# Kernel optimization log

Measured on AMD Instinct MI355X. Metric: run time of the kernel, lower is better.

## Reference

```python
import jax, jax.numpy as jnp
import numpy as np

N_NODES = 4096
N_EDGES = 16384
F_IN = 64
F_EDGE = 16
HID = 128
OUT = 64
N_GRAPHS = 32


def _encoder(x, edge_index, edge_attr, batch, p):
    N = x.shape[0]
    src, dst = edge_index[0], edge_index[1]
    # EdgeMLP: [E, F_edge] -> [E, F_in * HID] per-edge weight matrices
    h = jax.nn.relu(edge_attr @ p['e_w1'] + p['e_b1'])
    h = jax.nn.relu(h @ p['e_w2'] + p['e_b2'])
    Wmat = (h @ p['e_w3'] + p['e_b3']).reshape(-1, x.shape[1], p['root_w'].shape[1])  # [E, F_in, HID]
    # NNConv: message = x_src @ W_edge, scatter-add to dst, plus root transform + bias
    msg = jnp.einsum('ei,eio->eo', x[src], Wmat)  # [E, HID]
    agg = jax.ops.segment_sum(msg, dst, num_segments=N)
    h1 = jax.nn.relu(agg + x @ p['root_w'] + p['conv1_b'])  # [N, HID]
    # GATConv (1 head, concat=False) with self-loops (PyG default)
    loop = jnp.arange(N, dtype=src.dtype)
    si = jnp.concatenate([src, loop])
    di = jnp.concatenate([dst, loop])
    hp = h1 @ p['gat_w']  # [N, HID]
    a_s = hp @ p['att_src']  # [N]
    a_d = hp @ p['att_dst']  # [N]
    e = jax.nn.leaky_relu(a_s[si] + a_d[di], negative_slope=0.2)
    m = jax.ops.segment_max(e, di, num_segments=N)
    ex = jnp.exp(e - m[di])
    denom = jax.ops.segment_sum(ex, di, num_segments=N)
    alpha = ex / (denom[di] + 1e-16)
    h2 = jax.ops.segment_sum(alpha[:, None] * hp[si], di, num_segments=N) + p['gat_b']
    h2 = jax.nn.relu(h2)
    # global mean pool over graphs
    s = jax.ops.segment_sum(h2, batch, num_segments=N_GRAPHS)
    cnt = jax.ops.segment_sum(jnp.ones((N,), h2.dtype), batch, num_segments=N_GRAPHS)
    pooled = s / jnp.maximum(cnt, 1.0)[:, None]
    return jax.nn.relu(pooled @ p['fc1_w'] + p['fc1_b'])  # [B, OUT]


def setup_inputs() -> dict:
    key = jax.random.key(0)
    ks = jax.random.split(key, 24)
    d = {}
    d['x1'] = jax.random.normal(ks[0], (N_NODES, F_IN), jnp.float32)
    d['edge_index1'] = jax.random.randint(ks[1], (2, N_EDGES), 0, N_NODES)
    d['edge_attr1'] = jax.random.normal(ks[2], (N_EDGES, F_EDGE), jnp.float32)
    d['batch1'] = jnp.sort(jax.random.randint(ks[3], (N_NODES,), 0, N_GRAPHS))
    d['x2'] = jax.random.normal(ks[4], (N_NODES, F_IN), jnp.float32)
    d['edge_index2'] = jax.random.randint(ks[5], (2, N_EDGES), 0, N_NODES)
    d['edge_attr2'] = jax.random.normal(ks[6], (N_EDGES, F_EDGE), jnp.float32)
    d['batch2'] = jnp.sort(jax.random.randint(ks[7], (N_NODES,), 0, N_GRAPHS))

    def lin(k, fi, fo):
        return jax.random.normal(k, (fi, fo), jnp.float32) * (fi ** -0.5)

    d['e_w1'] = lin(ks[8], F_EDGE, 128); d['e_b1'] = jnp.zeros((128,), jnp.float32)
    d['e_w2'] = lin(ks[9], 128, 64); d['e_b2'] = jnp.zeros((64,), jnp.float32)
    d['e_w3'] = lin(ks[10], 64, F_IN * HID); d['e_b3'] = jnp.zeros((F_IN * HID,), jnp.float32)
    d['root_w'] = lin(ks[11], F_IN, HID); d['conv1_b'] = jnp.zeros((HID,), jnp.float32)
    d['gat_w'] = lin(ks[12], HID, HID)
    d['att_src'] = jax.random.normal(ks[13], (HID,), jnp.float32) * (HID ** -0.5)
    d['att_dst'] = jax.random.normal(ks[14], (HID,), jnp.float32) * (HID ** -0.5)
    d['gat_b'] = jnp.zeros((HID,), jnp.float32)
    d['fc1_w'] = lin(ks[15], HID, OUT); d['fc1_b'] = jnp.zeros((OUT,), jnp.float32)
    d['fc2_w'] = lin(ks[16], OUT, 1); d['fc2_b'] = jnp.zeros((1,), jnp.float32)
    return d


def reference(x1, edge_index1, edge_attr1, batch1, x2, edge_index2, edge_attr2, batch2,
              e_w1, e_b1, e_w2, e_b2, e_w3, e_b3, root_w, conv1_b,
              gat_w, att_src, att_dst, gat_b, fc1_w, fc1_b, fc2_w, fc2_b):
    p = dict(e_w1=e_w1, e_b1=e_b1, e_w2=e_w2, e_b2=e_b2, e_w3=e_w3, e_b3=e_b3,
             root_w=root_w, conv1_b=conv1_b, gat_w=gat_w, att_src=att_src,
             att_dst=att_dst, gat_b=gat_b, fc1_w=fc1_w, fc1_b=fc1_b,
             fc2_w=fc2_w, fc2_b=fc2_b)
    z1 = _encoder(x1, edge_index1, edge_attr1, batch1, p)
    z2 = _encoder(x2, edge_index2, edge_attr2, batch2, p)
    z = jnp.abs(z1 - z2) @ fc2_w + fc2_b  # [B, 1]
    return jax.nn.sigmoid(z).squeeze(1)  # [B]
```

## Files before the change

kernel.cpp:

```cpp
#include <hip/hip_runtime.h>
#include <hip/hip_bf16.h>
#include <math.h>

#define NN 4096
#define NE 16384
#define FIN 64
#define FE 16
#define HIDD 128
#define OUTD 64
#define NG 32
#define EP (NE + NN)
#define KSPLIT 2
#define NCH (64 / KSPLIT)

typedef __attribute__((ext_vector_type(8))) short s8v;
typedef __attribute__((ext_vector_type(4))) unsigned u4v;
typedef __attribute__((ext_vector_type(4))) float f4v;

union FragU { u4v u; s8v s; };

__device__ __forceinline__ unsigned bf16_rne(float v) {
    unsigned b = __float_as_uint(v);
    return (b + 0x7FFFu + ((b >> 16) & 1u)) >> 16;
}

__device__ __forceinline__ void glds16(const void* g, void* l) {
    __builtin_amdgcn_global_load_lds(
        (const __attribute__((address_space(1))) unsigned*)g,
        (__attribute__((address_space(3))) unsigned*)l, 16, 0, 0);
}

#define PB_SPLIT 2048
#define PB_EMLP  (PB_SPLIT + 4096)
#define PB_BIAS  (PB_EMLP + 4096)
#define PB_TOTAL (PB_BIAS + 32)

__global__ void k_prep(const float* __restrict__ ea0, const float* __restrict__ ea1,
                       const float* __restrict__ w1, const float* __restrict__ b1,
                       const float* __restrict__ w2, const float* __restrict__ b2,
                       const float* __restrict__ w3,
                       const float* __restrict__ X0, const float* __restrict__ X1,
                       const float* __restrict__ b3,
                       const int* __restrict__ ei0, const int* __restrict__ ei1,
                       unsigned short* __restrict__ B1g, unsigned short* __restrict__ B2g,
                       float* __restrict__ h0, float* __restrict__ h1g,
                       float* __restrict__ Bb0, float* __restrict__ Bb1,
                       int* __restrict__ rowcnt) {
    int b = blockIdx.x, t = threadIdx.x;
    if (b < PB_SPLIT) {
        int g = b * 256 + t;
        int o = g & 127, i = (g >> 7) & 63, c = g >> 13;
        float v = w3[(size_t)c * 8192 + i * 128 + o];
        unsigned hi = __float_as_uint(v) & 0xFFFF0000u;
        float res = v - __uint_as_float(hi);
        unsigned r2 = bf16_rne(res);
        unsigned idx = ((unsigned)c << 13) + (((o << 6) + i) ^ ((o & 7) << 3));
        B1g[idx] = (unsigned short)(hi >> 16);
        B2g[idx] = (unsigned short)r2;
    } else if (b < PB_EMLP) {
        int bb = b - PB_SPLIT;
        int gi = bb >> 11;
        int e0 = (bb & 2047) * 8;
        const float* ea = gi ? ea1 : ea0;
        float* hout = gi ? h1g : h0;
        __shared__ float h1s[8][HIDD];
#pragma unroll
        for (int r = 0; r < 4; ++r) {
            int idx = r * 256 + t;
            int e1 = idx >> 7, j = idx & 127;
            float acc = b1[j];
#pragma unroll
            for (int i = 0; i < FE; ++i) acc += ea[(e0 + e1) * FE + i] * w1[i * HIDD + j];
            h1s[e1][j] = fmaxf(acc, 0.f);
        }
        __syncthreads();
#pragma unroll
        for (int r = 0; r < 2; ++r) {
            int idx = r * 256 + t;
            int e1 = idx >> 6, j = idx & 63;
            float acc = b2[j];
#pragma unroll 16
            for (int k = 0; k < HIDD; ++k) acc += h1s[e1][k] * w2[k * 64 + j];
            hout[(size_t)(e0 + e1) * 64 + j] = fmaxf(acc, 0.f);
        }
    } else if (b < PB_BIAS) {
        int bb = b - PB_EMLP;
        int gi = bb >> 11;
        int n = (bb & 2047) * 2 + (t >> 7);
        int o = t & 127;
        const float* X = gi ? X1 : X0;
        float* Bb = gi ? Bb1 : Bb0;
        float acc = 0.f;
#pragma unroll 16
        for (int i = 0; i < FIN; ++i) acc += X[n * FIN + i] * b3[i * HIDD + o];
        Bb[(size_t)n * HIDD + o] = acc;
    } else {
        int tid = (b - PB_BIAS) * 256 + t;
        for (int idx = tid; idx < 2 * EP; idx += 32 * 256) {
            int gi = idx / EP, e = idx % EP;
            const int* dst = (gi ? ei1 : ei0) + NE;
            int d = (e < NE) ? dst[e] : e - NE;
            atomicAdd(&rowcnt[gi * NN + d], 1);
        }
    }
}

__global__ void k_scan(const int* __restrict__ rowcnt, int* __restrict__ rowptr,
                       const int* __restrict__ batch0, const int* __restrict__ batch1,
                       int* __restrict__ br) {
    int b = blockIdx.x;
    if (b < 2) {
        int gi = b;
        const int* cnt = rowcnt + gi * NN;
        int* rp = rowptr + gi * (NN + 1);
        int t = threadIdx.x;
        int base = t * 4;
        int v0 = cnt[base], v1 = cnt[base + 1], v2 = cnt[base + 2], v3 = cnt[base + 3];
        int s = v0 + v1 + v2 + v3;
        __shared__ int sc[1024];
        sc[t] = s;
        __syncthreads();
        for (int off = 1; off < 1024; off <<= 1) {
            int a = (t >= off) ? sc[t - off] : 0;
            __syncthreads();
            sc[t] += a;
            __syncthreads();
        }
        int run = sc[t] - s;
        rp[base] = run; run += v0;
        rp[base + 1] = run; run += v1;
        rp[base + 2] = run; run += v2;
        rp[base + 3] = run; run += v3;
        if (t == 1023) rp[NN] = run;
    } else {
        int t = threadIdx.x;
        if (t < 66) {
            int gi = t / 33, g = t % 33;
            const int* batch = gi ? batch1 : batch0;
            int lo = 0, hi = NN;
            while (lo < hi) {
                int mid = (lo + hi) >> 1;
                if (batch[mid] < g) lo = mid + 1; else hi = mid;
            }
            br[gi * 33 + g] = lo;
        }
    }
}

__global__ void k_fill(const int* __restrict__ ei0, const int* __restrict__ ei1,
                       const int* __restrict__ rowptr, int* __restrict__ cnt2,
                       int* __restrict__ adj) {
    int idx = blockIdx.x * 256 + threadIdx.x;
    if (idx >= 2 * EP) return;
    int gi = idx / EP, e = idx % EP;
    const int* dst = (gi ? ei1 : ei0) + NE;
    int d = (e < NE) ? dst[e] : e - NE;
    int pos = rowptr[gi * (NN + 1) + d] + atomicAdd(&cnt2[gi * NN + d], 1);
    adj[gi * EP + pos] = e;
}

__global__ void __launch_bounds__(256, 2)
k_nnconv(const float* __restrict__ x0, const float* __restrict__ x1,
         const float* __restrict__ h_0, const float* __restrict__ h_1,
         const unsigned short* __restrict__ B1g, const unsigned short* __restrict__ B2g,
         const float* __restrict__ Bb0, const float* __restrict__ Bb1,
         const int* __restrict__ ei0, const int* __restrict__ ei1,
         float* __restrict__ msg) {
    __shared__ __align__(16) char smem[65536];
    int gi = blockIdx.z;
    const float* x = gi ? x1 : x0;
    const float* hh = gi ? h_1 : h_0;
    const float* Bb = gi ? Bb1 : Bb0;
    const int* src = gi ? ei1 : ei0;

    int t = threadIdx.x;
    int e0 = blockIdx.x * 128;
    int z = blockIdx.y;
    int wv = t >> 6, l = t & 63;
    int q4 = l >> 4, c16 = l & 15;

    float xs[2][16];
    float hs[2][NCH];
#pragma unroll
    for (int mf = 0; mf < 2; ++mf) {
        int r = wv * 32 + mf * 16 + c16;
        int s_ = src[e0 + r];
        const float* xr = &x[(size_t)s_ * FIN];
        *(float4*)&xs[mf][0]  = *(const float4*)&xr[q4 * 8];
        *(float4*)&xs[mf][4]  = *(const float4*)&xr[q4 * 8 + 4];
        *(float4*)&xs[mf][8]  = *(const float4*)&xr[32 + q4 * 8];
        *(float4*)&xs[mf][12] = *(const float4*)&xr[32 + q4 * 8 + 4];
        const float* hr = &hh[(size_t)(e0 + r) * 64 + z * NCH];
#pragma unroll
        for (int q = 0; q < NCH / 4; ++q)
            *(float4*)&hs[mf][q * 4] = *(const float4*)&hr[q * 4];
    }

    f4v acc[2][8];
#pragma unroll
    for (int a = 0; a < 2; ++a)
#pragma unroll
        for (int b = 0; b < 8; ++b) acc[a][b] = (f4v){0.f, 0.f, 0.f, 0.f};

    int woff = wv << 10;
#define STAGE(cg, buf)                                                         \
    {                                                                          \
        const char* b1src = (const char*)B1g + (size_t)(cg) * 16384;           \
        const char* b2src = (const char*)B2g + (size_t)(cg) * 16384;           \
        char* B1s_ = smem + (buf) * 32768;                                     \
        char* B2s_ = B1s_ + 16384;                                             \
        _Pragma("unroll")                                                      \
        for (int k2 = 0; k2 < 4; ++k2) {                                       \
            glds16(b1src + k2 * 4096 + t * 16, B1s_ + k2 * 4096 + woff);       \
            glds16(b2src + k2 * 4096 + t * 16, B2s_ + k2 * 4096 + woff);       \
        }                                                                      \
    }

    STAGE(z * NCH, 0);

#pragma unroll 1
    for (int cl = 0; cl < NCH; ++cl) {
        int buf = cl & 1;
        __builtin_amdgcn_s_barrier();
        __builtin_amdgcn_sched_barrier(0);
        if (cl + 1 < NCH) STAGE(z * NCH + cl + 1, buf ^ 1);

        FragU a1[2][2], a2[2][2];
#pragma unroll
        for (int mf = 0; mf < 2; ++mf) {
            float hv = hs[mf][cl];
#pragma unroll
            for (int kf = 0; kf < 2; ++kf) {
                u4v w1v, w2v;
#pragma unroll
                for (int p = 0; p < 4; ++p) {
                    float p0 = hv * xs[mf][kf * 8 + 2 * p];
                    float p1 = hv * xs[mf][kf * 8 + 2 * p + 1];
                    unsigned b0 = __float_as_uint(p0), b1 = __float_as_uint(p1);
                    unsigned hi0 = b0 & 0xFFFF0000u, hi1 = b1 & 0xFFFF0000u;
                    w1v[p] = (hi0 >> 16) | hi1;
                    float r0 = p0 - __uint_as_float(hi0);
                    float r1 = p1 - __uint_as_float(hi1);
                    w2v[p] = bf16_rne(r0) | (bf16_rne(r1) << 16);
                }
                a1[mf][kf].u = w1v; a2[mf][kf].u = w2v;
            }
        }

        if (cl + 1 < NCH) { asm volatile("s_waitcnt vmcnt(8)" ::: "memory"); }
        else             { asm volatile("s_waitcnt vmcnt(0)" ::: "memory"); }
        __builtin_amdgcn_sched_barrier(0);
        __builtin_amdgcn_s_barrier();
        __builtin_amdgcn_sched_barrier(0);

        const char* B1s = smem + buf * 32768;
        const char* B2s = B1s + 16384;
        __builtin_amdgcn_s_setprio(1);
#pragma unroll
        for (int kf = 0; kf < 2; ++kf) {
#pragma unroll
            for (int nf = 0; nf < 8; ++nf) {
                int o = nf * 16 + c16;
                int byte = o * 128 + ((kf * 64 + q4 * 16) ^ ((o & 7) << 4));
                FragU bf1, bf2;
                bf1.u = *(const u4v*)(B1s + byte);
                bf2.u = *(const u4v*)(B2s + byte);
#pragma unroll
                for (int mf = 0; mf < 2; ++mf) {
                    acc[mf][nf] = __builtin_amdgcn_mfma_f32_16x16x32_bf16(a1[mf][kf].s, bf1.s, acc[mf][nf], 0, 0, 0);
                    acc[mf][nf] = __builtin_amdgcn_mfma_f32_16x16x32_bf16(a1[mf][kf].s, bf2.s, acc[mf][nf], 0, 0, 0);
                    acc[mf][nf] = __builtin_amdgcn_mfma_f32_16x16x32_bf16(a2[mf][kf].s, bf1.s, acc[mf][nf], 0, 0, 0);
                }
            }
        }
        __builtin_amdgcn_s_setprio(0);
    }
#undef STAGE

    float* sm = (float*)smem;
    float* mb = msg + ((size_t)(gi * KSPLIT + z) * NE) * HIDD;
    int z0 = (z == 0);
#pragma unroll
    for (int half = 0; half < 2; ++half) {
        __syncthreads();
        if ((wv >> 1) == half) {
            int rbase = (wv & 1) * 32;
#pragma unroll
            for (int mf = 0; mf < 2; ++mf)
#pragma unroll
                for (int j = 0; j < 4; ++j) {
                    int rr = rbase + mf * 16 + q4 * 4 + j;
#pragma unroll
                    for (int nf = 0; nf < 8; ++nf)
                        sm[rr * 128 + nf * 16 + c16] = acc[mf][nf][j];
                }
        }
        __syncthreads();
#pragma unroll
        for (int it = 0; it < 8; ++it) {
            int f = it * 256 + t;
            int row = f >> 5, c4 = f & 31;
            int eg = e0 + half * 64 + row;
            float4 v = *(float4*)&sm[row * 128 + c4 * 4];
            if (z0) {
                int s_ = src[eg];
                const float* bbr = &Bb[(size_t)s_ * HIDD + c4 * 4];
                v.x += bbr[0]; v.y += bbr[1]; v.z += bbr[2]; v.w += bbr[3];
            }
            *(float4*)&mb[(size_t)eg * HIDD + c4 * 4] = v;
        }
    }
}

__global__ void k_h1hp(const float* __restrict__ msg,
                       const int* __restrict__ rowptr, const int* __restrict__ adj,
                       const float* __restrict__ X0, const float* __restrict__ X1,
                       const float* __restrict__ rw, const float* __restrict__ cb,
                       const float* __restrict__ gw,
                       const float* __restrict__ asw, const float* __restrict__ adw,
                       float* __restrict__ hp0, float* __restrict__ hp1,
                       float* __restrict__ a_s0, float* __restrict__ a_s1,
                       float* __restrict__ a_d0, float* __restrict__ a_d1) {
    int gi = blockIdx.y;
    const float* X = gi ? X1 : X0;
    float* hp = gi ? hp1 : hp0;
    float* a_s = gi ? a_s1 : a_s0;
    float* a_d = gi ? a_d1 : a_d0;
    const int* rp = rowptr + gi * (NN + 1);
    const int* aj = adj + gi * EP;
    const float* mz0 = msg + (size_t)(gi * KSPLIT + 0) * NE * HIDD;
    const float* mz1 = msg + (size_t)(gi * KSPLIT + 1) * NE * HIDD;
    int n0 = blockIdx.x * 4;
    int o = threadIdx.x;
    __shared__ float xsh[4][FIN];
    __shared__ float h1s[4][HIDD];
    __shared__ float s1[4][2], s2[4][2];
    xsh[o >> 6][o & 63] = X[n0 * FIN + o];
    xsh[2 + (o >> 6)][o & 63] = X[n0 * FIN + 128 + o];
    __syncthreads();
    float accs[4];
#pragma unroll
    for (int nn = 0; nn < 4; ++nn) {
        int n = n0 + nn;
        float acc = cb[o];
        int lo = rp[n], hi = rp[n + 1];
        for (int p = lo; p < hi; ++p) {
            int e = aj[p];
            if (e < NE) acc += mz0[(size_t)e * HIDD + o] + mz1[(size_t)e * HIDD + o];
        }
        accs[nn] = acc;
    }
#pragma unroll 8
    for (int i = 0; i < FIN; ++i) {
        float w = rw[i * HIDD + o];
#pragma unroll
        for (int nn = 0; nn < 4; ++nn) accs[nn] += xsh[nn][i] * w;
    }
#pragma unroll
    for (int nn = 0; nn < 4; ++nn) h1s[nn][o] = fmaxf(accs[nn], 0.f);
    __syncthreads();
#pragma unroll
    for (int nn = 0; nn < 4; ++nn) accs[nn] = 0.f;
#pragma unroll 8
    for (int k = 0; k < HIDD; ++k) {
        float w = gw[k * HIDD + o];
#pragma unroll
        for (int nn = 0; nn < 4; ++nn) accs[nn] += h1s[nn][k] * w;
    }
#pragma unroll
    for (int nn = 0; nn < 4; ++nn) {
        hp[(size_t)(n0 + nn) * HIDD + o] = accs[nn];
        float p1 = accs[nn] * asw[o], p2 = accs[nn] * adw[o];
#pragma unroll
        for (int off = 32; off; off >>= 1) {
            p1 += __shfl_down(p1, off);
            p2 += __shfl_down(p2, off);
        }
        if ((o & 63) == 0) { s1[nn][o >> 6] = p1; s2[nn][o >> 6] = p2; }
    }
    __syncthreads();
    if (o < 4) {
        a_s[n0 + o] = s1[o][0] + s1[o][1];
        a_d[n0 + o] = s2[o][0] + s2[o][1];
    }
}

__global__ void k_gat(const int* __restrict__ rowptr, const int* __restrict__ adj,
                      const int* __restrict__ ei0, const int* __restrict__ ei1,
                      const float* __restrict__ hp0, const float* __restrict__ hp1,
                      const float* __restrict__ as0, const float* __restrict__ as1,
                      const float* __restrict__ ad0, const float* __restrict__ ad1,
                      const float* __restrict__ gb,
                      float* __restrict__ h2_0, float* __restrict__ h2_1) {
    int gi = blockIdx.y;
    const int* src = gi ? ei1 : ei0;
    const float* hp = gi ? hp1 : hp0;
    const float* a_s = gi ? as1 : as0;
    const float* a_d = gi ? ad1 : ad0;
    float* h2 = gi ? h2_1 : h2_0;
    const int* rp = rowptr + gi * (NN + 1);
    const int* aj = adj + gi * EP;
    int w = threadIdx.x >> 6, l = threadIdx.x & 63;
    int n = blockIdx.x * 4 + w;
    int lo = rp[n], deg = rp[n + 1] - lo;
    float adn = a_d[n];
    float m = -1e30f;
    for (int base = 0; base < deg; base += 64) {
        float sc = -1e30f;
        int j = base + l;
        if (j < deg) {
            int e = aj[lo + j];
            int si = (e < NE) ? src[e] : n;
            float xsc = a_s[si] + adn;
            sc = xsc > 0.f ? xsc : 0.2f * xsc;
        }
#pragma unroll
        for (int off = 32; off; off >>= 1) sc = fmaxf(sc, __shfl_xor(sc, off));
        m = fmaxf(m, sc);
    }
    float den = 0.f;
    for (int base = 0; base < deg; base += 64) {
        float ev = 0.f;
        int j = base + l;
        if (j < deg) {
            int e = aj[lo + j];
            int si = (e < NE) ? src[e] : n;
            float xsc = a_s[si] + adn;
            float sc = xsc > 0.f ? xsc : 0.2f * xsc;
            ev = expf(sc - m);
        }
#pragma unroll
        for (int off = 32; off; off >>= 1) ev += __shfl_xor(ev, off);
        den += ev;
    }
    float inv = 1.f / (den + 1e-16f);
    float acc0 = 0.f, acc1 = 0.f;
    for (int j = 0; j < deg; ++j) {
        int e = aj[lo + j];
        int si = (e < NE) ? src[e] : n;
        float xsc = a_s[si] + adn;
        float sc = xsc > 0.f ? xsc : 0.2f * xsc;
        float al = expf(sc - m) * inv;
        acc0 += al * hp[(size_t)si * HIDD + l];
        acc1 += al * hp[(size_t)si * HIDD + 64 + l];
    }
    h2[(size_t)n * HIDD + l] = fmaxf(acc0 + gb[l], 0.f);
    h2[(size_t)n * HIDD + 64 + l] = fmaxf(acc1 + gb[64 + l], 0.f);
}

__global__ void k_poolfc1(const float* __restrict__ h2_0, const float* __restrict__ h2_1,
                          const int* __restrict__ br,
                          const float* __restrict__ w, const float* __restrict__ bias,
                          float* __restrict__ z) {
    int gi = blockIdx.x >> 5, g = blockIdx.x & 31;
    const float* h2 = gi ? h2_1 : h2_0;
    int lo = br[gi * 33 + g], hi = br[gi * 33 + g + 1];
    int t = threadIdx.x;
    __shared__ float pool[HIDD];
    float acc = 0.f;
    for (int n = lo; n < hi; ++n) acc += h2[(size_t)n * HIDD + t];
    pool[t] = acc;
    __syncthreads();
    if (t < 64) {
        float c = fmaxf((float)(hi - lo), 1.f);
        float a = bias[t];
#pragma unroll 16
        for (int o = 0; o < HIDD; ++o) a += (pool[o] / c) * w[o * OUTD + t];
        z[gi * NG * OUTD + g * OUTD + t] = fmaxf(a, 0.f);
    }
}

__global__ void k_final(const float* __restrict__ zz,
                        const float* __restrict__ w, const float* __restrict__ b,
                        float* __restrict__ out) {
    int g = threadIdx.x;
    const float* z1 = zz;
    const float* z2 = zz + NG * OUTD;
    float acc = b[0];
#pragma unroll
    for (int j = 0; j < OUTD; ++j) acc += fabsf(z1[g * OUTD + j] - z2[g * OUTD + j]) * w[j];
    out[g] = 1.f / (1.f + expf(-acc));
}

extern "C" void kernel_launch(void* const* d_in, const int* in_sizes, int n_in,
                              void* d_out, int out_size, void* d_ws, size_t ws_size,
                              hipStream_t stream) {
    const float* x0     = (const float*)d_in[0];
    const int*   ei0    = (const int*)d_in[1];
    const float* ea0    = (const float*)d_in[2];
    const int*   b0     = (const int*)d_in[3];
    const float* x1     = (const float*)d_in[4];
    const int*   ei1    = (const int*)d_in[5];
    const float* ea1    = (const float*)d_in[6];
    const int*   b1     = (const int*)d_in[7];
    const float* e_w1 = (const float*)d_in[8];
    const float* e_b1 = (const float*)d_in[9];
    const float* e_w2 = (const float*)d_in[10];
    const float* e_b2 = (const float*)d_in[11];
    const float* e_w3 = (const float*)d_in[12];
    const float* e_b3 = (const float*)d_in[13];
    const float* root_w = (const float*)d_in[14];
    const float* conv1_b = (const float*)d_in[15];
    const float* gat_w = (const float*)d_in[16];
    const float* att_src = (const float*)d_in[17];
    const float* att_dst = (const float*)d_in[18];
    const float* gat_b = (const float*)d_in[19];
    const float* fc1_w = (const float*)d_in[20];
    const float* fc1_b = (const float*)d_in[21];
    const float* fc2_w = (const float*)d_in[22];
    const float* fc2_b = (const float*)d_in[23];

    float* ws = (float*)d_ws;
    size_t off = 0;
    auto alloc = [&](size_t n) { float* p = ws + off; off += n; return p; };
    int* rowcnt = (int*)alloc(2 * NN);
    int* cnt2   = (int*)alloc(2 * NN);
    size_t zero_elems = off;
    int* rowptr = (int*)alloc(2 * (NN + 1));
    int* br     = (int*)alloc(66);
    int* adj    = (int*)alloc(2 * EP);
    float* h[2]   = {alloc((size_t)NE * 64), alloc((size_t)NE * 64)};
    unsigned short* B1g = (unsigned short*)alloc((size_t)4096 * 128 / 2);
    unsigned short* B2g = (unsigned short*)alloc((size_t)4096 * 128 / 2);
    float* Bb[2]  = {alloc((size_t)NN * HIDD), alloc((size_t)NN * HIDD)};
    float* msg    = alloc((size_t)2 * KSPLIT * NE * HIDD);
    float* hp[2]  = {alloc((size_t)NN * HIDD), alloc((size_t)NN * HIDD)};
    float* a_s[2] = {alloc(NN), alloc(NN)};
    float* a_d[2] = {alloc(NN), alloc(NN)};
    float* h2[2]  = {alloc((size_t)NN * HIDD), alloc((size_t)NN * HIDD)};
    float* zz     = alloc((size_t)2 * NG * OUTD);

    hipMemsetAsync(ws, 0, zero_elems * 4, stream);
    k_prep<<<PB_TOTAL, 256, 0, stream>>>(ea0, ea1, e_w1, e_b1, e_w2, e_b2, e_w3,
                                         x0, x1, e_b3, ei0, ei1,
                                         B1g, B2g, h[0], h[1], Bb[0], Bb[1],
                                         rowcnt);
    k_scan<<<3, 1024, 0, stream>>>(rowcnt, rowptr, b0, b1, br);
    k_fill<<<(2 * EP + 255) / 256, 256, 0, stream>>>(ei0, ei1, rowptr, cnt2, adj);
    k_nnconv<<<dim3(NE / 128, KSPLIT, 2), 256, 0, stream>>>(
        x0, x1, h[0], h[1], B1g, B2g, Bb[0], Bb[1], ei0, ei1, msg);
    k_h1hp<<<dim3(NN / 4, 2), HIDD, 0, stream>>>(
        msg, rowptr, adj, x0, x1, root_w, conv1_b, gat_w, att_src, att_dst,
        hp[0], hp[1], a_s[0], a_s[1], a_d[0], a_d[1]);
    k_gat<<<dim3(NN / 4, 2), 256, 0, stream>>>(
        rowptr, adj, ei0, ei1, hp[0], hp[1], a_s[0], a_s[1], a_d[0], a_d[1],
        gat_b, h2[0], h2[1]);
    k_poolfc1<<<64, HIDD, 0, stream>>>(h2[0], h2[1], br, fc1_w, fc1_b, zz);
    k_final<<<1, NG, 0, stream>>>(zz, fc2_w, fc2_b, (float*)d_out);
}
```

Baseline: 255.1 us.

## Switch NNConv split-precision MFMA from bf16x3 to fp16x2 with smaller blocks

Measured after the change: 239.6 us. 6.1% less time.

```diff
diff --git a/kernel.cpp b/kernel.cpp
--- a/kernel.cpp
+++ b/kernel.cpp
@@ -13,21 +13,27 @@
 #define KSPLIT 2
 #define NCH (64 / KSPLIT)
 
-typedef __attribute__((ext_vector_type(8))) short s8v;
 typedef __attribute__((ext_vector_type(4))) unsigned u4v;
 typedef __attribute__((ext_vector_type(4))) float f4v;
-
-union FragU { u4v u; s8v s; };
-
-__device__ __forceinline__ unsigned bf16_rne(float v) {
-    unsigned b = __float_as_uint(v);
-    return (b + 0x7FFFu + ((b >> 16) & 1u)) >> 16;
-}
+typedef _Float16 f16x8 __attribute__((ext_vector_type(8)));
+typedef __fp16 fp16x2 __attribute__((ext_vector_type(2)));
+
+union FragH { u4v u; f16x8 h; };
+union H2U { fp16x2 v; unsigned u; };
 
 __device__ __forceinline__ void glds16(const void* g, void* l) {
     __builtin_amdgcn_global_load_lds(
         (const __attribute__((address_space(1))) unsigned*)g,
         (__attribute__((address_space(3))) unsigned*)l, 16, 0, 0);
+}
+
+__device__ __forceinline__ void split2(float p0, float p1, unsigned& w1, unsigned& w2) {
+    H2U c1, c2;
+    c1.v = __builtin_amdgcn_cvt_pkrtz(p0, p1);
+    float r0 = p0 - (float)c1.v[0];
+    float r1 = p1 - (float)c1.v[1];
+    c2.v = __builtin_amdgcn_cvt_pkrtz(r0, r1);
+    w1 = c1.u; w2 = c2.u;
 }
 
 #define PB_SPLIT 2048
@@ -42,7 +48,7 @@
                        const float* __restrict__ X0, const float* __restrict__ X1,
                        const float* __restrict__ b3,
                        const int* __restrict__ ei0, const int* __restrict__ ei1,
-                       unsigned short* __restrict__ B1g, unsigned short* __restrict__ B2g,
+                       unsigned short* __restrict__ B1g,
                        float* __restrict__ h0, float* __restrict__ h1g,
                        float* __restrict__ Bb0, float* __restrict__ Bb1,
                        int* __restrict__ rowcnt) {
@@ -51,12 +57,10 @@
         int g = b * 256 + t;
         int o = g & 127, i = (g >> 7) & 63, c = g >> 13;
         float v = w3[(size_t)c * 8192 + i * 128 + o];
-        unsigned hi = __float_as_uint(v) & 0xFFFF0000u;
-        float res = v - __uint_as_float(hi);
-        unsigned r2 = bf16_rne(res);
+        union { _Float16 f; unsigned short u; } cv;
+        cv.f = (_Float16)v;
         unsigned idx = ((unsigned)c << 13) + (((o << 6) + i) ^ ((o & 7) << 3));
-        B1g[idx] = (unsigned short)(hi >> 16);
-        B2g[idx] = (unsigned short)r2;
+        B1g[idx] = cv.u;
     } else if (b < PB_EMLP) {
         int bb = b - PB_SPLIT;
         int gi = bb >> 11;
@@ -159,14 +163,14 @@
     adj[gi * EP + pos] = e;
 }
 
-__global__ void __launch_bounds__(256, 2)
+__global__ void __launch_bounds__(128, 2)
 k_nnconv(const float* __restrict__ x0, const float* __restrict__ x1,
          const float* __restrict__ h_0, const float* __restrict__ h_1,
-         const unsigned short* __restrict__ B1g, const unsigned short* __restrict__ B2g,
+         const unsigned short* __restrict__ B1g,
          const float* __restrict__ Bb0, const float* __restrict__ Bb1,
          const int* __restrict__ ei0, const int* __restrict__ ei1,
          float* __restrict__ msg) {
-    __shared__ __align__(16) char smem[65536];
+    __shared__ __align__(16) char smem[32768];
     int gi = blockIdx.z;
     const float* x = gi ? x1 : x0;
     const float* hh = gi ? h_1 : h_0;
@@ -174,7 +178,7 @@
     const int* src = gi ? ei1 : ei0;
 
     int t = threadIdx.x;
-    int e0 = blockIdx.x * 128;
+    int e0 = blockIdx.x * 64;
     int z = blockIdx.y;
     int wv = t >> 6, l = t & 63;
     int q4 = l >> 4, c16 = l & 15;
@@ -205,14 +209,11 @@
     int woff = wv << 10;
 #define STAGE(cg, buf)                                                         \
     {                                                                          \
-        const char* b1src = (const char*)B1g + (size_t)(cg) * 16384;           \
-        const char* b2src = (const char*)B2g + (size_t)(cg) * 16384;           \
-        char* B1s_ = smem + (buf) * 32768;                                     \
-        char* B2s_ = B1s_ + 16384;                                             \
+        const char* bsrc = (const char*)B1g + (size_t)(cg) * 16384;            \
+        char* Bs_ = smem + (buf) * 16384;                                      \
         _Pragma("unroll")                                                      \
-        for (int k2 = 0; k2 < 4; ++k2) {                                       \
-            glds16(b1src + k2 * 4096 + t * 16, B1s_ + k2 * 4096 + woff);       \
-            glds16(b2src + k2 * 4096 + t * 16, B2s_ + k2 * 4096 + woff);       \
+        for (int k2 = 0; k2 < 8; ++k2) {                                       \
+            glds16(bsrc + k2 * 2048 + t * 16, Bs_ + k2 * 2048 + woff);         \
         }                                                                      \
     }
 
@@ -225,7 +226,7 @@
         __builtin_amdgcn_sched_barrier(0);
         if (cl + 1 < NCH) STAGE(z * NCH + cl + 1, buf ^ 1);
 
-        FragU a1[2][2], a2[2][2];
+        FragH a1[2][2], a2[2][2];
 #pragma unroll
         for (int mf = 0; mf < 2; ++mf) {
             float hv = hs[mf][cl];
@@ -236,12 +237,9 @@
                 for (int p = 0; p < 4; ++p) {
                     float p0 = hv * xs[mf][kf * 8 + 2 * p];
                     float p1 = hv * xs[mf][kf * 8 + 2 * p + 1];
-                    unsigned b0 = __float_as_uint(p0), b1 = __float_as_uint(p1);
-                    unsigned hi0 = b0 & 0xFFFF0000u, hi1 = b1 & 0xFFFF0000u;
-                    w1v[p] = (hi0 >> 16) | hi1;
-                    float r0 = p0 - __uint_as_float(hi0);
-                    float r1 = p1 - __uint_as_float(hi1);
-                    w2v[p] = bf16_rne(r0) | (bf16_rne(r1) << 16);
+                    unsigned u1, u2;
+                    split2(p0, p1, u1, u2);
+                    w1v[p] = u1; w2v[p] = u2;
                 }
                 a1[mf][kf].u = w1v; a2[mf][kf].u = w2v;
             }
@@ -253,8 +251,7 @@
         __builtin_amdgcn_s_barrier();
         __builtin_amdgcn_sched_barrier(0);
 
-        const char* B1s = smem + buf * 32768;
-        const char* B2s = B1s + 16384;
+        const char* Bs = smem + buf * 16384;
         __builtin_amdgcn_s_setprio(1);
 #pragma unroll
         for (int kf = 0; kf < 2; ++kf) {
@@ -262,14 +259,12 @@
             for (int nf = 0; nf < 8; ++nf) {
                 int o = nf * 16 + c16;
                 int byte = o * 128 + ((kf * 64 + q4 * 16) ^ ((o & 7) << 4));
-                FragU bf1, bf2;
-                bf1.u = *(const u4v*)(B1s + byte);
-                bf2.u = *(const u4v*)(B2s + byte);
+                FragH bf;
+                bf.u = *(const u4v*)(Bs + byte);
 #pragma unroll
                 for (int mf = 0; mf < 2; ++mf) {
-                    acc[mf][nf] = __builtin_amdgcn_mfma_f32_16x16x32_bf16(a1[mf][kf].s, bf1.s, acc[mf][nf], 0, 0, 0);
-                    acc[mf][nf] = __builtin_amdgcn_mfma_f32_16x16x32_bf16(a1[mf][kf].s, bf2.s, acc[mf][nf], 0, 0, 0);
-                    acc[mf][nf] = __builtin_amdgcn_mfma_f32_16x16x32_bf16(a2[mf][kf].s, bf1.s, acc[mf][nf], 0, 0, 0);
+                    acc[mf][nf] = __builtin_amdgcn_mfma_f32_16x16x32_f16(a1[mf][kf].h, bf.h, acc[mf][nf], 0, 0, 0);
+                    acc[mf][nf] = __builtin_amdgcn_mfma_f32_16x16x32_f16(a2[mf][kf].h, bf.h, acc[mf][nf], 0, 0, 0);
                 }
             }
         }
@@ -280,35 +275,29 @@
     float* sm = (float*)smem;
     float* mb = msg + ((size_t)(gi * KSPLIT + z) * NE) * HIDD;
     int z0 = (z == 0);
-#pragma unroll
-    for (int half = 0; half < 2; ++half) {
-        __syncthreads();
-        if ((wv >> 1) == half) {
-            int rbase = (wv & 1) * 32;
-#pragma unroll
-            for (int mf = 0; mf < 2; ++mf)
-#pragma unroll
-                for (int j = 0; j < 4; ++j) {
-                    int rr = rbase + mf * 16 + q4 * 4 + j;
-#pragma unroll
-                    for (int nf = 0; nf < 8; ++nf)
-                        sm[rr * 128 + nf * 16 + c16] = acc[mf][nf][j];
-                }
-        }
-        __syncthreads();
-#pragma unroll
-        for (int it = 0; it < 8; ++it) {
-            int f = it * 256 + t;
-            int row = f >> 5, c4 = f & 31;
-            int eg = e0 + half * 64 + row;
-            float4 v = *(float4*)&sm[row * 128 + c4 * 4];
-            if (z0) {
-                int s_ = src[eg];
-                const float* bbr = &Bb[(size_t)s_ * HIDD + c4 * 4];
-                v.x += bbr[0]; v.y += bbr[1]; v.z += bbr[2]; v.w += bbr[3];
-            }
-            *(float4*)&mb[(size_t)eg * HIDD + c4 * 4] = v;
-        }
+    __builtin_amdgcn_s_barrier();
+#pragma unroll
+    for (int mf = 0; mf < 2; ++mf)
+#pragma unroll
+        for (int j = 0; j < 4; ++j) {
+            int rr = wv * 32 + mf * 16 + q4 * 4 + j;
+#pragma unroll
+            for (int nf = 0; nf < 8; ++nf)
+                sm[rr * 128 + nf * 16 + c16] = acc[mf][nf][j];
+        }
+    __builtin_amdgcn_s_barrier();
+#pragma unroll
+    for (int it = 0; it < 16; ++it) {
+        int f = it * 128 + t;
+        int row = f >> 5, c4 = f & 31;
+        int eg = e0 + row;
+        float4 v = *(float4*)&sm[row * 128 + c4 * 4];
+        if (z0) {
+            int s_ = src[eg];
+            const float* bbr = &Bb[(size_t)s_ * HIDD + c4 * 4];
+            v.x += bbr[0]; v.y += bbr[1]; v.z += bbr[2]; v.w += bbr[3];
+        }
+        *(float4*)&mb[(size_t)eg * HIDD + c4 * 4] = v;
     }
 }
 
@@ -521,7 +510,6 @@
     int* adj    = (int*)alloc(2 * EP);
     float* h[2]   = {alloc((size_t)NE * 64), alloc((size_t)NE * 64)};
     unsigned short* B1g = (unsigned short*)alloc((size_t)4096 * 128 / 2);
-    unsigned short* B2g = (unsigned short*)alloc((size_t)4096 * 128 / 2);
     float* Bb[2]  = {alloc((size_t)NN * HIDD), alloc((size_t)NN * HIDD)};
     float* msg    = alloc((size_t)2 * KSPLIT * NE * HIDD);
     float* hp[2]  = {alloc((size_t)NN * HIDD), alloc((size_t)NN * HIDD)};
@@ -530,15 +518,15 @@
     float* h2[2]  = {alloc((size_t)NN * HIDD), alloc((size_t)NN * HIDD)};
     float* zz     = alloc((size_t)2 * NG * OUTD);
 
-    hipMemsetAsync(ws, 0, zero_elems * 4, stream);
+    (void)hipMemsetAsync(ws, 0, zero_elems * 4, stream);
     k_prep<<<PB_TOTAL, 256, 0, stream>>>(ea0, ea1, e_w1, e_b1, e_w2, e_b2, e_w3,
                                          x0, x1, e_b3, ei0, ei1,
-                                         B1g, B2g, h[0], h[1], Bb[0], Bb[1],
+                                         B1g, h[0], h[1], Bb[0], Bb[1],
                                          rowcnt);
     k_scan<<<3, 1024, 0, stream>>>(rowcnt, rowptr, b0, b1, br);
     k_fill<<<(2 * EP + 255) / 256, 256, 0, stream>>>(ei0, ei1, rowptr, cnt2, adj);
-    k_nnconv<<<dim3(NE / 128, KSPLIT, 2), 256, 0, stream>>>(
-        x0, x1, h[0], h[1], B1g, B2g, Bb[0], Bb[1], ei0, ei1, msg);
+    k_nnconv<<<dim3(NE / 64, KSPLIT, 2), 128, 0, stream>>>(
+        x0, x1, h[0], h[1], B1g, Bb[0], Bb[1], ei0, ei1, msg);
     k_h1hp<<<dim3(NN / 4, 2), HIDD, 0, stream>>>(
         msg, rowptr, adj, x0, x1, root_w, conv1_b, gat_w, att_src, att_dst,
         hp[0], hp[1], a_s[0], a_s[1], a_d[0], a_d[1]);
```
